# Kernel optimization log

Hardware: AMD Instinct MI355X
Metric: run time of the kernel (lower is better)

## Reference

```python
import jax, jax.numpy as jnp
import numpy as np

NUM_HEADS = 32
NUM_KV_GROUPS = 8
HEAD_DIM = 64  # dim_out // num_heads
DIM_IN = 2048
DIM_OUT = 2048


def setup_inputs() -> dict:
    key = jax.random.key(0)
    k_x, k_q, k_k, k_v, k_o = jax.random.split(key, 5)
    s = 0.02
    x = jax.random.normal(k_x, (1, 2048, DIM_IN), dtype=jnp.float32)
    wq = jax.random.normal(k_q, (DIM_IN, DIM_OUT), dtype=jnp.float32) * s
    wk = jax.random.normal(k_k, (DIM_IN, NUM_KV_GROUPS * HEAD_DIM), dtype=jnp.float32) * s
    wv = jax.random.normal(k_v, (DIM_IN, NUM_KV_GROUPS * HEAD_DIM), dtype=jnp.float32) * s
    wo = jax.random.normal(k_o, (DIM_OUT, DIM_OUT), dtype=jnp.float32) * s
    return {"x": x, "wq": wq, "wk": wk, "wv": wv, "wo": wo}


def reference(x, wq, wk, wv, wo):
    b, n, _ = x.shape
    g, r, d = NUM_KV_GROUPS, NUM_HEADS // NUM_KV_GROUPS, HEAD_DIM
    # projections
    q = (x @ wq).reshape(b, n, g, r, d)          # [b,n,g,r,d] heads grouped
    k = (x @ wk).reshape(b, n, g, d)             # [b,n,g,d]
    v = (x @ wv).reshape(b, n, g, d)
    # scores: repeat_interleave of K over group dim == broadcast over r
    scores = jnp.einsum('bqgrd,bkgd->bgrqk', q, k)  # [b,g,r,n,n]
    causal = jnp.tril(jnp.ones((n, n), dtype=bool))
    scores = jnp.where(causal, scores, -jnp.inf)
    attn = jax.nn.softmax(scores / jnp.sqrt(jnp.asarray(d, x.dtype)), axis=-1)
    ctx = jnp.einsum('bgrqk,bkgd->bqgrd', attn, v)  # [b,n,g,r,d]
    out = ctx.reshape(b, n, g * r * d) @ wo
    return out
```

## Files before the change

kernel.cpp:

```cpp
#include <hip/hip_runtime.h>


typedef __attribute__((ext_vector_type(8))) short bf16x8;
typedef __attribute__((ext_vector_type(4))) short bf16x4;
typedef __attribute__((ext_vector_type(4))) float f32x4;

__device__ __forceinline__ short f2bf(float f) {
  unsigned u = __builtin_bit_cast(unsigned, f);
  u += 0x7FFFu + ((u >> 16) & 1u);
  return (short)(u >> 16);
}

__device__ __forceinline__ unsigned pkbf(float a, float b) {
  const unsigned ua = __builtin_bit_cast(unsigned, a) + 0x8000u;
  const unsigned ub = __builtin_bit_cast(unsigned, b) + 0x8000u;
  return __builtin_amdgcn_perm(ub, ua, 0x07060302u);
}

__device__ __forceinline__ void gload_lds16(const void* g, void* l) {
  __builtin_amdgcn_global_load_lds(
      (const __attribute__((address_space(1))) unsigned int*)g,
      (__attribute__((address_space(3))) unsigned int*)l, 16, 0, 0);
}

__global__ __launch_bounds__(256) void cvtx(const float* __restrict__ x,
                                            short* __restrict__ y) {
  const int i = (blockIdx.x * 256 + threadIdx.x) * 4;
  const float4 v = *(const float4*)&x[i];
  bf16x4 r;
  r[0] = f2bf(v.x); r[1] = f2bf(v.y); r[2] = f2bf(v.z); r[3] = f2bf(v.w);
  *(bf16x4*)&y[i] = r;
}

__global__ __launch_bounds__(256) void tcvt4(const float* __restrict__ wq,
                                             const float* __restrict__ wk,
                                             const float* __restrict__ wv,
                                             const float* __restrict__ wo,
                                             short* __restrict__ dq,
                                             short* __restrict__ dk,
                                             short* __restrict__ dv,
                                             short* __restrict__ dwo) {
  const int z = blockIdx.z;
  const float* src;
  short* dst;
  int C;
  if (z == 0)      { src = wq; dst = dq;  C = 2048; }
  else if (z == 1) { src = wk; dst = dk;  C = 512; }
  else if (z == 2) { src = wv; dst = dv;  C = 512; }
  else             { src = wo; dst = dwo; C = 2048; }
  const int c0 = blockIdx.x * 32;
  if (c0 >= C) return;
  const int R = 2048;
  __shared__ float t[32][33];
  const int r0 = blockIdx.y * 32;
  const int tx = threadIdx.x & 31, ty = threadIdx.x >> 5;
#pragma unroll
  for (int i = 0; i < 4; ++i)
    t[ty + i * 8][tx] = src[(r0 + ty + i * 8) * C + c0 + tx];
  __syncthreads();
#pragma unroll
  for (int i = 0; i < 4; ++i)
    dst[(c0 + ty + i * 8) * R + r0 + tx] = f2bf(t[tx][ty + i * 8]);
}

__global__ __launch_bounds__(256) void tbf(const short* __restrict__ src,
                                           short* __restrict__ dst,
                                           int R, int C, int ldsrc) {
  __shared__ short t[32][33];
  const int c0 = blockIdx.x * 32, r0 = blockIdx.y * 32;
  const int tx = threadIdx.x & 31, ty = threadIdx.x >> 5;
#pragma unroll
  for (int i = 0; i < 4; ++i)
    t[ty + i * 8][tx] = src[(r0 + ty + i * 8) * ldsrc + c0 + tx];
  __syncthreads();
#pragma unroll
  for (int i = 0; i < 4; ++i)
    dst[(c0 + ty + i * 8) * R + r0 + tx] = t[tx][ty + i * 8];
}

template <int OUT_BF16, int BN>
__global__ __launch_bounds__(128) void gemm_bt(const short* __restrict__ A,
                                               const short* __restrict__ B,
                                               void* __restrict__ Cv,
                                               int M, int N, int K,
                                               float cscale, int scale_cols) {
  __shared__ short As[2][64 * 64];
  __shared__ short Bs[2][BN * 64];
  const int tid = threadIdx.x;
  const int lane = tid & 63, wid = tid >> 6;
  const int l15 = lane & 15, lg = lane >> 4;
  const int lr = lane >> 3, lc = lane & 7;
  const int row0 = blockIdx.y * 64, col0 = blockIdx.x * BN;
  const int sswz = l15 & 7;
  f32x4 acc[4][BN / 32] = {};
  const int arow = wid * 8 + lr;
  const short* ag = A + (row0 + arow) * K + (lc ^ lr) * 8;
  const short* bg = B + (col0 + arow) * K + (lc ^ lr) * 8;

  auto stage = [&](int b, int kk) {
    short* lA = &As[b][wid * 512];
    short* lB = &Bs[b][wid * 512];
#pragma unroll
    for (int c = 0; c < 4; ++c)
      gload_lds16(ag + c * 16 * K + kk, lA + c * 1024);
#pragma unroll
    for (int c = 0; c < BN / 16; ++c)
      gload_lds16(bg + c * 16 * K + kk, lB + c * 1024);
  };

  stage(0, 0);
  __syncthreads();
  const int nb = K / 64;
  int buf = 0;
  for (int t = 0; t < nb; ++t) {
    if (t + 1 < nb) stage(buf ^ 1, (t + 1) * 64);
#pragma unroll
    for (int x = 0; x < 2; ++x) {
      bf16x8 af[4], bfr[BN / 32];
#pragma unroll
      for (int m = 0; m < 4; ++m)
        af[m] = *(const bf16x8*)&As[buf][(m * 16 + l15) * 64 + (((x * 4 + lg) ^ sswz) * 8)];
#pragma unroll
      for (int n = 0; n < BN / 32; ++n)
        bfr[n] = *(const bf16x8*)&Bs[buf][(wid * (BN / 2) + n * 16 + l15) * 64 + (((x * 4 + lg) ^ sswz) * 8)];
#pragma unroll
      for (int m = 0; m < 4; ++m)
#pragma unroll
        for (int n = 0; n < BN / 32; ++n)
          acc[m][n] = __builtin_amdgcn_mfma_f32_16x16x32_bf16(af[m], bfr[n],
                                                              acc[m][n], 0, 0, 0);
    }
    __syncthreads();
    buf ^= 1;
  }
#pragma unroll
  for (int m = 0; m < 4; ++m)
#pragma unroll
    for (int n = 0; n < BN / 32; ++n)
#pragma unroll
      for (int i = 0; i < 4; ++i) {
        const int r = row0 + m * 16 + lg * 4 + i;
        const int c = col0 + wid * (BN / 2) + n * 16 + l15;
        float v = acc[m][n][i];
        if (c < scale_cols) v *= cscale;
        if (OUT_BF16)
          ((short*)Cv)[r * N + c] = f2bf(v);
        else
          ((float*)Cv)[r * N + c] = v;
      }
}

__global__ __launch_bounds__(256) void attn_fwd(const short* __restrict__ QKV,
                                                const short* __restrict__ Vt,
                                                short* __restrict__ CTX) {
  const int ldq = 3072;
  const int qb = 31 - (int)blockIdx.x;
  const int hp = blockIdx.y;
  const int g = hp >> 1;
  const int h0 = g * 4 + (hp & 1) * 2;
  const int lane = threadIdx.x & 63, wid = threadIdx.x >> 6;
  const int l15 = lane & 15, lg = lane >> 4;
  const int qrow0 = qb * 64 + wid * 16;

  __shared__ short Ks[2][64 * 64];
  __shared__ short Vs[2][64 * 64];
  __shared__ short Ps[4][2][16 * 64];

  const int swz = (l15 & 7) << 3;

  bf16x8 qf[2][2];
#pragma unroll
  for (int hh = 0; hh < 2; ++hh)
#pragma unroll
    for (int kc = 0; kc < 2; ++kc)
      qf[hh][kc] = *(const bf16x8*)&QKV[(qrow0 + l15) * ldq + (h0 + hh) * 64 + kc * 32 + lg * 8];

  float l_run[2] = {0.f, 0.f};
  f32x4 accO[2][4] = {};

  const int srow = threadIdx.x >> 3, sseg = threadIdx.x & 7;
  const int ssw = (sseg ^ (srow & 7)) * 8;
  const short* Kg = QKV + 2048 + g * 64 + sseg * 8;
  const short* Vg = Vt + (g * 64 + srow) * 2048 + sseg * 8;

  bf16x8 rk0 = *(const bf16x8*)&Kg[srow * ldq];
  bf16x8 rk1 = *(const bf16x8*)&Kg[(srow + 32) * ldq];
  bf16x8 rv0 = *(const bf16x8*)&Vg[0];
  bf16x8 rv1 = *(const bf16x8*)&Vg[32 * 2048];

  for (int kt = 0; kt <= qb; ++kt) {
    const int buf = kt & 1;
    const int tokbase = kt * 64;
    *(bf16x8*)&Ks[buf][srow * 64 + ssw] = rk0;
    *(bf16x8*)&Ks[buf][(srow + 32) * 64 + ssw] = rk1;
    *(bf16x8*)&Vs[buf][srow * 64 + ssw] = rv0;
    *(bf16x8*)&Vs[buf][(srow + 32) * 64 + ssw] = rv1;
    if (kt < qb) {
      const int nb = (kt + 1) * 64;
      rk0 = *(const bf16x8*)&Kg[(nb + srow) * ldq];
      rk1 = *(const bf16x8*)&Kg[(nb + srow + 32) * ldq];
      rv0 = *(const bf16x8*)&Vg[nb];
      rv1 = *(const bf16x8*)&Vg[32 * 2048 + nb];
    }
    __syncthreads();

    f32x4 s[2][4];
    __builtin_amdgcn_s_setprio(1);
#pragma unroll
    for (int t = 0; t < 4; ++t) {
      s[0][t] = (f32x4){0.f, 0.f, 0.f, 0.f};
      s[1][t] = (f32x4){0.f, 0.f, 0.f, 0.f};
#pragma unroll
      for (int kc = 0; kc < 2; ++kc) {
        const bf16x8 kf =
            *(const bf16x8*)&Ks[buf][(t * 16 + l15) * 64 + (((kc * 4 + lg) ^ (l15 & 7)) * 8)];
        s[0][t] = __builtin_amdgcn_mfma_f32_16x16x32_bf16(kf, qf[0][kc], s[0][t], 0, 0, 0);
        s[1][t] = __builtin_amdgcn_mfma_f32_16x16x32_bf16(kf, qf[1][kc], s[1][t], 0, 0, 0);
      }
    }
    __builtin_amdgcn_s_setprio(0);

    if (kt == qb) {
      const int kq = tokbase + lg * 4 - qrow0 - l15;
#pragma unroll
      for (int t = 0; t < 4; ++t)
#pragma unroll
        for (int i = 0; i < 4; ++i)
          if (kq + t * 16 + i > 0) { s[0][t][i] = -3e38f; s[1][t][i] = -3e38f; }
    }

#pragma unroll
    for (int hh = 0; hh < 2; ++hh) {
      float ts[4];
#pragma unroll
      for (int t = 0; t < 4; ++t) {
        const float e0 = __builtin_amdgcn_exp2f(s[hh][t][0]);
        const float e1 = __builtin_amdgcn_exp2f(s[hh][t][1]);
        const float e2 = __builtin_amdgcn_exp2f(s[hh][t][2]);
        const float e3 = __builtin_amdgcn_exp2f(s[hh][t][3]);
        s[hh][t][0] = e0; s[hh][t][1] = e1; s[hh][t][2] = e2; s[hh][t][3] = e3;
        ts[t] = (e0 + e1) + (e2 + e3);
      }
      float rs = (ts[0] + ts[1]) + (ts[2] + ts[3]);
      rs += __shfl_xor(rs, 16);
      rs += __shfl_xor(rs, 32);
      l_run[hh] += rs;
    }

#pragma unroll
    for (int t = 0; t < 4; ++t) {
      uint2 w0, w1;
      w0.x = pkbf(s[0][t][0], s[0][t][1]); w0.y = pkbf(s[0][t][2], s[0][t][3]);
      w1.x = pkbf(s[1][t][0], s[1][t][1]); w1.y = pkbf(s[1][t][2], s[1][t][3]);
      *(uint2*)&Ps[wid][0][l15 * 64 + ((t * 16 + lg * 4) ^ swz)] = w0;
      *(uint2*)&Ps[wid][1][l15 * 64 + ((t * 16 + lg * 4) ^ swz)] = w1;
    }
    __builtin_amdgcn_s_setprio(1);
#pragma unroll
    for (int kc = 0; kc < 2; ++kc) {
      const bf16x8 pb0 =
          *(const bf16x8*)&Ps[wid][0][l15 * 64 + ((kc * 32 + lg * 8) ^ swz)];
      const bf16x8 pb1 =
          *(const bf16x8*)&Ps[wid][1][l15 * 64 + ((kc * 32 + lg * 8) ^ swz)];
#pragma unroll
      for (int t2 = 0; t2 < 4; ++t2) {
        const bf16x8 vb =
            *(const bf16x8*)&Vs[buf][(t2 * 16 + l15) * 64 + (((kc * 4 + lg) ^ (l15 & 7)) * 8)];
        accO[0][t2] = __builtin_amdgcn_mfma_f32_16x16x32_bf16(vb, pb0, accO[0][t2], 0, 0, 0);
        accO[1][t2] = __builtin_amdgcn_mfma_f32_16x16x32_bf16(vb, pb1, accO[1][t2], 0, 0, 0);
      }
    }
    __builtin_amdgcn_s_setprio(0);
  }

#pragma unroll
  for (int hh = 0; hh < 2; ++hh) {
    const float inv = 1.0f / l_run[hh];
#pragma unroll
    for (int t2 = 0; t2 < 4; ++t2) {
      bf16x4 w;
#pragma unroll
      for (int i = 0; i < 4; ++i) w[i] = f2bf(accO[hh][t2][i] * inv);
      *(bf16x4*)&Ps[wid][hh][l15 * 64 + ((t2 * 16 + lg * 4) ^ swz)] = w;
    }
#pragma unroll
    for (int r = 0; r < 2; ++r) {
      const int seg = lg + r * 4;
      const bf16x8 row = *(const bf16x8*)&Ps[wid][hh][l15 * 64 + ((seg * 8) ^ swz)];
      *(bf16x8*)&CTX[(qrow0 + l15) * 2048 + (h0 + hh) * 64 + seg * 8] = row;
    }
  }
}

extern "C" void kernel_launch(void* const* d_in, const int* in_sizes, int n_in,
                              void* d_out, int out_size, void* d_ws, size_t ws_size,
                              hipStream_t stream) {
  (void)in_sizes; (void)n_in; (void)out_size; (void)ws_size;
  const float* x  = (const float*)d_in[0];
  const float* wq = (const float*)d_in[1];
  const float* wk = (const float*)d_in[2];
  const float* wv = (const float*)d_in[3];
  const float* wo = (const float*)d_in[4];
  float* out = (float*)d_out;

  char* ws = (char*)d_ws;
  short* Xb  = (short*)(ws);
  short* WT  = (short*)(ws + 8388608);
  short* WoT = (short*)(ws + 20971520);
  short* QKV = (short*)(ws + 29360128);
  short* Vt  = (short*)(ws + 41943040);
  short* CTX = (short*)(ws + 44040192);

  const float qscale = 0.125f * 1.4426950408889634f;

  cvtx<<<4096, 256, 0, stream>>>(x, Xb);
  { dim3 g(64, 64, 4);
    tcvt4<<<g, 256, 0, stream>>>(wq, wk, wv, wo,
                                 WT, WT + 2048 * 2048, WT + 2560 * 2048, WoT); }
  { dim3 g(32, 32); gemm_bt<1, 96><<<g, 128, 0, stream>>>(Xb, WT, QKV, 2048, 3072, 2048, qscale, 2048); }
  { dim3 g(16, 64); tbf<<<g, 256, 0, stream>>>(QKV + 2560, Vt, 2048, 512, 3072); }
  { dim3 g(32, 16); attn_fwd<<<g, 256, 0, stream>>>(QKV, Vt, CTX); }
  { dim3 g(32, 32); gemm_bt<0, 64><<<g, 128, 0, stream>>>(CTX, WoT, out, 2048, 2048, 2048, 1.0f, 0); }
}
```

Baseline: 134.0 us.

## Split KV range across two warp groups, pair causal Q blocks, use permlane P fragments

The attention kernel now runs 512 threads as two 4-wave groups. Each group processes alternating KV tiles for the same Q block, and the partial O and l are merged through shared memory. Each block handles a complementary pair of Q blocks (31-b and b) to balance the causal work, which halves the grid. The P matrix is moved into MFMA B-operand layout with permlane32/16 swaps instead of a round trip through LDS. This trades fewer blocks, more LDS and an extra reduction step for shorter serial KV loops and less LDS traffic per tile.

```diff
diff --git a/kernel.cpp b/kernel.cpp
--- a/kernel.cpp
+++ b/kernel.cpp
@@ -4,6 +4,7 @@
 typedef __attribute__((ext_vector_type(8))) short bf16x8;
 typedef __attribute__((ext_vector_type(4))) short bf16x4;
 typedef __attribute__((ext_vector_type(4))) float f32x4;
+typedef __attribute__((ext_vector_type(4))) unsigned u32x4;
 
 __device__ __forceinline__ short f2bf(float f) {
   unsigned u = __builtin_bit_cast(unsigned, f);
@@ -15,6 +16,25 @@
   const unsigned ua = __builtin_bit_cast(unsigned, a) + 0x8000u;
   const unsigned ub = __builtin_bit_cast(unsigned, b) + 0x8000u;
   return __builtin_amdgcn_perm(ub, ua, 0x07060302u);
+}
+
+__device__ __forceinline__ void pswap(unsigned a, unsigned b,
+                                      unsigned& r0, unsigned& r1) {
+  auto t = __builtin_amdgcn_permlane32_swap(a, b, false, false);
+  auto u = __builtin_amdgcn_permlane16_swap(t[0], t[1], false, false);
+  r0 = u[0]; r1 = u[1];
+}
+
+__device__ __forceinline__ void build_bfrag(const f32x4* sv, bf16x8& b0, bf16x8& b1) {
+  const unsigned c0 = pkbf(sv[0][0], sv[0][1]), d0 = pkbf(sv[0][2], sv[0][3]);
+  const unsigned c1 = pkbf(sv[1][0], sv[1][1]), d1 = pkbf(sv[1][2], sv[1][3]);
+  const unsigned c2 = pkbf(sv[2][0], sv[2][1]), d2 = pkbf(sv[2][2], sv[2][3]);
+  const unsigned c3 = pkbf(sv[3][0], sv[3][1]), d3 = pkbf(sv[3][2], sv[3][3]);
+  unsigned q0, q1, q2, q3, r0, r1, r2, r3;
+  pswap(c0, c1, q0, q2); pswap(d0, d1, q1, q3);
+  pswap(c2, c3, r0, r2); pswap(d2, d3, r1, r3);
+  b0 = __builtin_bit_cast(bf16x8, (u32x4){q0, q1, q2, q3});
+  b1 = __builtin_bit_cast(bf16x8, (u32x4){r0, r1, r2, r3});
 }
 
 __device__ __forceinline__ void gload_lds16(const void* g, void* l) {
@@ -150,144 +170,171 @@
       }
 }
 
-__global__ __launch_bounds__(256) void attn_fwd(const short* __restrict__ QKV,
+__global__ __launch_bounds__(512) void attn_fwd(const short* __restrict__ QKV,
                                                 const short* __restrict__ Vt,
                                                 short* __restrict__ CTX) {
   const int ldq = 3072;
-  const int qb = 31 - (int)blockIdx.x;
-  const int hp = blockIdx.y;
+  const int hp = blockIdx.x;
+  const int bxp = blockIdx.y;
   const int g = hp >> 1;
   const int h0 = g * 4 + (hp & 1) * 2;
-  const int lane = threadIdx.x & 63, wid = threadIdx.x >> 6;
+  const int tid = threadIdx.x;
+  const int lane = tid & 63, wid = tid >> 6;
+  const int grp = wid >> 2;
+  const int wq = wid & 3;
   const int l15 = lane & 15, lg = lane >> 4;
-  const int qrow0 = qb * 64 + wid * 16;
-
-  __shared__ short Ks[2][64 * 64];
-  __shared__ short Vs[2][64 * 64];
-  __shared__ short Ps[4][2][16 * 64];
-
-  const int swz = (l15 & 7) << 3;
-
-  bf16x8 qf[2][2];
-#pragma unroll
-  for (int hh = 0; hh < 2; ++hh)
-#pragma unroll
-    for (int kc = 0; kc < 2; ++kc)
-      qf[hh][kc] = *(const bf16x8*)&QKV[(qrow0 + l15) * ldq + (h0 + hh) * 64 + kc * 32 + lg * 8];
-
-  float l_run[2] = {0.f, 0.f};
-  f32x4 accO[2][4] = {};
-
-  const int srow = threadIdx.x >> 3, sseg = threadIdx.x & 7;
+
+  __shared__ short Ks[2][2][64 * 64];
+  __shared__ short Vs[2][2][64 * 64];
+  __shared__ float CB[4][64][36];
+
+  const int ltid = tid & 255;
+  const int srow = ltid >> 3, sseg = ltid & 7;
   const int ssw = (sseg ^ (srow & 7)) * 8;
   const short* Kg = QKV + 2048 + g * 64 + sseg * 8;
   const short* Vg = Vt + (g * 64 + srow) * 2048 + sseg * 8;
 
-  bf16x8 rk0 = *(const bf16x8*)&Kg[srow * ldq];
-  bf16x8 rk1 = *(const bf16x8*)&Kg[(srow + 32) * ldq];
-  bf16x8 rv0 = *(const bf16x8*)&Vg[0];
-  bf16x8 rv1 = *(const bf16x8*)&Vg[32 * 2048];
-
-  for (int kt = 0; kt <= qb; ++kt) {
-    const int buf = kt & 1;
-    const int tokbase = kt * 64;
-    *(bf16x8*)&Ks[buf][srow * 64 + ssw] = rk0;
-    *(bf16x8*)&Ks[buf][(srow + 32) * 64 + ssw] = rk1;
-    *(bf16x8*)&Vs[buf][srow * 64 + ssw] = rv0;
-    *(bf16x8*)&Vs[buf][(srow + 32) * 64 + ssw] = rv1;
-    if (kt < qb) {
-      const int nb = (kt + 1) * 64;
-      rk0 = *(const bf16x8*)&Kg[(nb + srow) * ldq];
-      rk1 = *(const bf16x8*)&Kg[(nb + srow + 32) * ldq];
-      rv0 = *(const bf16x8*)&Vg[nb];
-      rv1 = *(const bf16x8*)&Vg[32 * 2048 + nb];
+  bf16x8 rk0, rk1, rv0, rv1;
+  {
+    const int tb = grp * 64;
+    rk0 = *(const bf16x8*)&Kg[(tb + srow) * ldq];
+    rk1 = *(const bf16x8*)&Kg[(tb + srow + 32) * ldq];
+    rv0 = *(const bf16x8*)&Vg[tb];
+    rv1 = *(const bf16x8*)&Vg[32 * 2048 + tb];
+  }
+
+#pragma unroll 1
+  for (int half = 0; half < 2; ++half) {
+    const int qb = half ? bxp : 31 - bxp;
+    const int qrow0 = qb * 64 + wq * 16;
+
+    bf16x8 qf[2][2];
+#pragma unroll
+    for (int hh = 0; hh < 2; ++hh)
+#pragma unroll
+      for (int kc = 0; kc < 2; ++kc)
+        qf[hh][kc] = *(const bf16x8*)&QKV[(qrow0 + l15) * ldq + (h0 + hh) * 64 + kc * 32 + lg * 8];
+
+    float l_run[2] = {0.f, 0.f};
+    f32x4 accO[2][4] = {};
+
+    const int nint = (qb >> 1) + 1;
+#pragma unroll 1
+    for (int j = 0; j < nint; ++j) {
+      const int kt = 2 * j + grp;
+      const bool valid = kt <= qb;
+      const int buf = j & 1;
+      if (valid) {
+        *(bf16x8*)&Ks[grp][buf][srow * 64 + ssw] = rk0;
+        *(bf16x8*)&Ks[grp][buf][(srow + 32) * 64 + ssw] = rk1;
+        *(bf16x8*)&Vs[grp][buf][srow * 64 + ssw] = rv0;
+        *(bf16x8*)&Vs[grp][buf][(srow + 32) * 64 + ssw] = rv1;
+      }
+      if (kt + 2 <= qb) {
+        const int nb = (kt + 2) * 64;
+        rk0 = *(const bf16x8*)&Kg[(nb + srow) * ldq];
+        rk1 = *(const bf16x8*)&Kg[(nb + srow + 32) * ldq];
+        rv0 = *(const bf16x8*)&Vg[nb];
+        rv1 = *(const bf16x8*)&Vg[32 * 2048 + nb];
+      }
+      __syncthreads();
+      if (!valid) continue;
+
+      const int tokbase = kt * 64;
+      f32x4 s[2][4];
+      __builtin_amdgcn_s_setprio(1);
+#pragma unroll
+      for (int t = 0; t < 4; ++t) {
+        s[0][t] = (f32x4){0.f, 0.f, 0.f, 0.f};
+        s[1][t] = (f32x4){0.f, 0.f, 0.f, 0.f};
+#pragma unroll
+        for (int kc = 0; kc < 2; ++kc) {
+          const bf16x8 kf =
+              *(const bf16x8*)&Ks[grp][buf][(t * 16 + l15) * 64 + (((kc * 4 + lg) ^ (l15 & 7)) * 8)];
+          s[0][t] = __builtin_amdgcn_mfma_f32_16x16x32_bf16(kf, qf[0][kc], s[0][t], 0, 0, 0);
+          s[1][t] = __builtin_amdgcn_mfma_f32_16x16x32_bf16(kf, qf[1][kc], s[1][t], 0, 0, 0);
+        }
+      }
+      __builtin_amdgcn_s_setprio(0);
+
+      if (kt == qb) {
+        const int kq = tokbase + lg * 4 - qrow0 - l15;
+#pragma unroll
+        for (int t = 0; t < 4; ++t)
+#pragma unroll
+          for (int i = 0; i < 4; ++i)
+            if (kq + t * 16 + i > 0) { s[0][t][i] = -3e38f; s[1][t][i] = -3e38f; }
+      }
+
+#pragma unroll
+      for (int hh = 0; hh < 2; ++hh) {
+        float ts = 0.f;
+#pragma unroll
+        for (int t = 0; t < 4; ++t) {
+          const float e0 = __builtin_amdgcn_exp2f(s[hh][t][0]);
+          const float e1 = __builtin_amdgcn_exp2f(s[hh][t][1]);
+          const float e2 = __builtin_amdgcn_exp2f(s[hh][t][2]);
+          const float e3 = __builtin_amdgcn_exp2f(s[hh][t][3]);
+          s[hh][t][0] = e0; s[hh][t][1] = e1; s[hh][t][2] = e2; s[hh][t][3] = e3;
+          ts += (e0 + e1) + (e2 + e3);
+        }
+        ts += __shfl_xor(ts, 16);
+        ts += __shfl_xor(ts, 32);
+        l_run[hh] += ts;
+      }
+
+      bf16x8 pb[2][2];
+      build_bfrag(s[0], pb[0][0], pb[0][1]);
+      build_bfrag(s[1], pb[1][0], pb[1][1]);
+
+      __builtin_amdgcn_s_setprio(1);
+#pragma unroll
+      for (int kc = 0; kc < 2; ++kc)
+#pragma unroll
+        for (int t2 = 0; t2 < 4; ++t2) {
+          const bf16x8 vb =
+              *(const bf16x8*)&Vs[grp][buf][(t2 * 16 + l15) * 64 + (((kc * 4 + lg) ^ (l15 & 7)) * 8)];
+          accO[0][t2] = __builtin_amdgcn_mfma_f32_16x16x32_bf16(vb, pb[0][kc], accO[0][t2], 0, 0, 0);
+          accO[1][t2] = __builtin_amdgcn_mfma_f32_16x16x32_bf16(vb, pb[1][kc], accO[1][t2], 0, 0, 0);
+        }
+      __builtin_amdgcn_s_setprio(0);
+    }
+
+    if (half == 0 && grp <= bxp) {
+      const int tb = grp * 64;
+      rk0 = *(const bf16x8*)&Kg[(tb + srow) * ldq];
+      rk1 = *(const bf16x8*)&Kg[(tb + srow + 32) * ldq];
+      rv0 = *(const bf16x8*)&Vg[tb];
+      rv1 = *(const bf16x8*)&Vg[32 * 2048 + tb];
+    }
+
+    if (grp == 1) {
+#pragma unroll
+      for (int hh = 0; hh < 2; ++hh)
+#pragma unroll
+        for (int t2 = 0; t2 < 4; ++t2)
+          *(f32x4*)&CB[wq][lane][hh * 16 + t2 * 4] = accO[hh][t2];
+      *(float2*)&CB[wq][lane][32] = make_float2(l_run[0], l_run[1]);
     }
     __syncthreads();
-
-    f32x4 s[2][4];
-    __builtin_amdgcn_s_setprio(1);
-#pragma unroll
-    for (int t = 0; t < 4; ++t) {
-      s[0][t] = (f32x4){0.f, 0.f, 0.f, 0.f};
-      s[1][t] = (f32x4){0.f, 0.f, 0.f, 0.f};
-#pragma unroll
-      for (int kc = 0; kc < 2; ++kc) {
-        const bf16x8 kf =
-            *(const bf16x8*)&Ks[buf][(t * 16 + l15) * 64 + (((kc * 4 + lg) ^ (l15 & 7)) * 8)];
-        s[0][t] = __builtin_amdgcn_mfma_f32_16x16x32_bf16(kf, qf[0][kc], s[0][t], 0, 0, 0);
-        s[1][t] = __builtin_amdgcn_mfma_f32_16x16x32_bf16(kf, qf[1][kc], s[1][t], 0, 0, 0);
-      }
-    }
-    __builtin_amdgcn_s_setprio(0);
-
-    if (kt == qb) {
-      const int kq = tokbase + lg * 4 - qrow0 - l15;
-#pragma unroll
-      for (int t = 0; t < 4; ++t)
-#pragma unroll
-        for (int i = 0; i < 4; ++i)
-          if (kq + t * 16 + i > 0) { s[0][t][i] = -3e38f; s[1][t][i] = -3e38f; }
-    }
-
-#pragma unroll
-    for (int hh = 0; hh < 2; ++hh) {
-      float ts[4];
-#pragma unroll
-      for (int t = 0; t < 4; ++t) {
-        const float e0 = __builtin_amdgcn_exp2f(s[hh][t][0]);
-        const float e1 = __builtin_amdgcn_exp2f(s[hh][t][1]);
-        const float e2 = __builtin_amdgcn_exp2f(s[hh][t][2]);
-        const float e3 = __builtin_amdgcn_exp2f(s[hh][t][3]);
-        s[hh][t][0] = e0; s[hh][t][1] = e1; s[hh][t][2] = e2; s[hh][t][3] = e3;
-        ts[t] = (e0 + e1) + (e2 + e3);
-      }
-      float rs = (ts[0] + ts[1]) + (ts[2] + ts[3]);
-      rs += __shfl_xor(rs, 16);
-      rs += __shfl_xor(rs, 32);
-      l_run[hh] += rs;
-    }
-
-#pragma unroll
-    for (int t = 0; t < 4; ++t) {
-      uint2 w0, w1;
-      w0.x = pkbf(s[0][t][0], s[0][t][1]); w0.y = pkbf(s[0][t][2], s[0][t][3]);
-      w1.x = pkbf(s[1][t][0], s[1][t][1]); w1.y = pkbf(s[1][t][2], s[1][t][3]);
-      *(uint2*)&Ps[wid][0][l15 * 64 + ((t * 16 + lg * 4) ^ swz)] = w0;
-      *(uint2*)&Ps[wid][1][l15 * 64 + ((t * 16 + lg * 4) ^ swz)] = w1;
-    }
-    __builtin_amdgcn_s_setprio(1);
-#pragma unroll
-    for (int kc = 0; kc < 2; ++kc) {
-      const bf16x8 pb0 =
-          *(const bf16x8*)&Ps[wid][0][l15 * 64 + ((kc * 32 + lg * 8) ^ swz)];
-      const bf16x8 pb1 =
-          *(const bf16x8*)&Ps[wid][1][l15 * 64 + ((kc * 32 + lg * 8) ^ swz)];
-#pragma unroll
-      for (int t2 = 0; t2 < 4; ++t2) {
-        const bf16x8 vb =
-            *(const bf16x8*)&Vs[buf][(t2 * 16 + l15) * 64 + (((kc * 4 + lg) ^ (l15 & 7)) * 8)];
-        accO[0][t2] = __builtin_amdgcn_mfma_f32_16x16x32_bf16(vb, pb0, accO[0][t2], 0, 0, 0);
-        accO[1][t2] = __builtin_amdgcn_mfma_f32_16x16x32_bf16(vb, pb1, accO[1][t2], 0, 0, 0);
-      }
-    }
-    __builtin_amdgcn_s_setprio(0);
-  }
-
-#pragma unroll
-  for (int hh = 0; hh < 2; ++hh) {
-    const float inv = 1.0f / l_run[hh];
-#pragma unroll
-    for (int t2 = 0; t2 < 4; ++t2) {
-      bf16x4 w;
-#pragma unroll
-      for (int i = 0; i < 4; ++i) w[i] = f2bf(accO[hh][t2][i] * inv);
-      *(bf16x4*)&Ps[wid][hh][l15 * 64 + ((t2 * 16 + lg * 4) ^ swz)] = w;
-    }
-#pragma unroll
-    for (int r = 0; r < 2; ++r) {
-      const int seg = lg + r * 4;
-      const bf16x8 row = *(const bf16x8*)&Ps[wid][hh][l15 * 64 + ((seg * 8) ^ swz)];
-      *(bf16x8*)&CTX[(qrow0 + l15) * 2048 + (h0 + hh) * 64 + seg * 8] = row;
+    if (grp == 0) {
+      const float2 lcb = *(const float2*)&CB[wq][lane][32];
+#pragma unroll
+      for (int hh = 0; hh < 2; ++hh) {
+        const float lt = l_run[hh] + (hh ? lcb.y : lcb.x);
+        const float inv = 1.0f / lt;
+        f32x4 ov[4];
+#pragma unroll
+        for (int t2 = 0; t2 < 4; ++t2) {
+          const f32x4 cb = *(const f32x4*)&CB[wq][lane][hh * 16 + t2 * 4];
+#pragma unroll
+          for (int i = 0; i < 4; ++i) ov[t2][i] = (accO[hh][t2][i] + cb[i]) * inv;
+        }
+        bf16x8 ob0, ob1;
+        build_bfrag(ov, ob0, ob1);
+        *(bf16x8*)&CTX[(qrow0 + l15) * 2048 + (h0 + hh) * 64 + lg * 8] = ob0;
+        *(bf16x8*)&CTX[(qrow0 + l15) * 2048 + (h0 + hh) * 64 + 32 + lg * 8] = ob1;
+      }
     }
   }
 }
@@ -319,6 +366,6 @@
                                  WT, WT + 2048 * 2048, WT + 2560 * 2048, WoT); }
   { dim3 g(32, 32); gemm_bt<1, 96><<<g, 128, 0, stream>>>(Xb, WT, QKV, 2048, 3072, 2048, qscale, 2048); }
   { dim3 g(16, 64); tbf<<<g, 256, 0, stream>>>(QKV + 2560, Vt, 2048, 512, 3072); }
-  { dim3 g(32, 16); attn_fwd<<<g, 256, 0, stream>>>(QKV, Vt, CTX); }
+  { dim3 g(16, 16); attn_fwd<<<g, 512, 0, stream>>>(QKV, Vt, CTX); }
   { dim3 g(32, 32); gemm_bt<0, 64><<<g, 128, 0, stream>>>(CTX, WoT, out, 2048, 2048, 2048, 1.0f, 0); }
 }
```

Result: faster. 118.8 us (-11.4%).
